# Optimization experiments

Measured on AMD Instinct MI355X. Metric: run time of the kernel, lower is better.

## Reference

```python
import jax, jax.numpy as jnp
import numpy as np

QUALITY = 95
X_MIN, X_MAX = 0.0, 1.0

# JPEG Annex K base quantization tables
_LUMA = np.array([
    [16, 11, 10, 16, 24, 40, 51, 61],
    [12, 12, 14, 19, 26, 58, 60, 55],
    [14, 13, 16, 24, 40, 57, 69, 56],
    [14, 17, 22, 29, 51, 87, 80, 62],
    [18, 22, 37, 56, 68, 109, 103, 77],
    [24, 35, 55, 64, 81, 104, 113, 92],
    [49, 64, 78, 87, 103, 121, 120, 101],
    [72, 92, 95, 98, 112, 100, 103, 99]], dtype=np.float32)
_CHROMA = np.array([
    [17, 18, 24, 47, 99, 99, 99, 99],
    [18, 21, 26, 66, 99, 99, 99, 99],
    [24, 26, 56, 99, 99, 99, 99, 99],
    [47, 66, 99, 99, 99, 99, 99, 99],
    [99, 99, 99, 99, 99, 99, 99, 99],
    [99, 99, 99, 99, 99, 99, 99, 99],
    [99, 99, 99, 99, 99, 99, 99, 99],
    [99, 99, 99, 99, 99, 99, 99, 99]], dtype=np.float32)

def _qtable(base, quality):
    # libjpeg quality scaling (quality >= 50 branch)
    scale = 5000.0 / quality if quality < 50 else 200.0 - 2.0 * quality
    return np.clip(np.floor((base * scale + 50.0) / 100.0), 1.0, 255.0).astype(np.float32)

_QL = jnp.asarray(_qtable(_LUMA, QUALITY))
_QC = jnp.asarray(_qtable(_CHROMA, QUALITY))

# Orthonormal 8x8 DCT-II matrix
_k = np.arange(8)
_D = np.sqrt(2.0 / 8.0) * np.cos((2 * _k[None, :] + 1) * _k[:, None] * np.pi / 16.0)
_D[0, :] /= np.sqrt(2.0)
_D = jnp.asarray(_D.astype(np.float32))

def _jpeg_channel(ch, table):
    """8x8 block DCT -> quantize(round) -> dequantize -> IDCT. ch: [B,H,W] level-shifted."""
    B, H, W = ch.shape
    xb = ch.reshape(B, H // 8, 8, W // 8, 8)
    coef = jnp.einsum('ki,bhiwj,lj->bhkwl', _D, xb, _D)
    t = table[None, None, :, None, :]
    deq = jnp.round(coef / t) * t
    rec = jnp.einsum('ki,bhkwl,lj->bhiwj', _D, deq, _D)
    return rec.reshape(B, H, W)

def _jpeg_roundtrip(x255):
    """x255: [B,H,W,3] float values in [0,255]. Simulates JPEG encode+decode (4:2:0)."""
    r, g, b = x255[..., 0], x255[..., 1], x255[..., 2]
    # JFIF RGB -> YCbCr
    y = 0.299 * r + 0.587 * g + 0.114 * b
    cb = -0.168736 * r - 0.331264 * g + 0.5 * b + 128.0
    cr = 0.5 * r - 0.418688 * g - 0.081312 * b + 128.0
    # Luma at full resolution
    y2 = _jpeg_channel(y - 128.0, _QL) + 128.0
    # Chroma: 2x2 average downsample (4:2:0), codec, nearest upsample
    def down(c):
        B, H, W = c.shape
        return c.reshape(B, H // 2, 2, W // 2, 2).mean(axis=(2, 4))
    def up(c):
        return jnp.repeat(jnp.repeat(c, 2, axis=1), 2, axis=2)
    cb2 = up(_jpeg_channel(down(cb) - 128.0, _QC) + 128.0)
    cr2 = up(_jpeg_channel(down(cr) - 128.0, _QC) + 128.0)
    # YCbCr -> RGB
    r2 = y2 + 1.402 * (cr2 - 128.0)
    g2 = y2 - 0.344136 * (cb2 - 128.0) - 0.714136 * (cr2 - 128.0)
    b2 = y2 + 1.772 * (cb2 - 128.0)
    rgb = jnp.stack([r2, g2, b2], axis=-1)
    return jnp.round(jnp.clip(rgb, 0.0, 255.0))  # decoded uint8 values


def setup_inputs() -> dict:
    key = jax.random.key(0)
    x = jax.random.uniform(key, (32, 512, 512, 3), dtype=jnp.float32)
    return {"x": x}


def reference(x):
    # inputs -> uint8 pixel values (tf.cast truncation; values are >= 0)
    x255 = jnp.clip(jnp.floor((x - X_MIN) / ((X_MAX - X_MIN) / 255.0)), 0.0, 255.0)
    dec = _jpeg_roundtrip(x255)
    # back to input range/dtype
    return dec / (255.0 / (X_MAX - X_MIN)) + X_MIN
```

## Files before the change

### kernel.cpp

```cpp
#include <hip/hip_runtime.h>
#include <cstddef>

static constexpr float D8[8][8] = {
  { 0.35355339059327373f, 0.35355339059327373f, 0.35355339059327373f, 0.35355339059327373f,
    0.35355339059327373f, 0.35355339059327373f, 0.35355339059327373f, 0.35355339059327373f},
  { 0.4903926402016152f,  0.4157348061512726f,  0.27778511650980114f, 0.09754516100806417f,
   -0.09754516100806417f,-0.27778511650980114f,-0.4157348061512726f, -0.4903926402016152f},
  { 0.46193976625564337f, 0.19134171618254492f,-0.19134171618254492f,-0.46193976625564337f,
   -0.46193976625564337f,-0.19134171618254492f, 0.19134171618254492f, 0.46193976625564337f},
  { 0.4157348061512726f, -0.09754516100806417f,-0.4903926402016152f, -0.27778511650980114f,
    0.27778511650980114f, 0.4903926402016152f,  0.09754516100806417f,-0.4157348061512726f},
  { 0.35355339059327373f,-0.35355339059327373f,-0.35355339059327373f, 0.35355339059327373f,
    0.35355339059327373f,-0.35355339059327373f,-0.35355339059327373f, 0.35355339059327373f},
  { 0.27778511650980114f,-0.4903926402016152f,  0.09754516100806417f, 0.4157348061512726f,
   -0.4157348061512726f, -0.09754516100806417f, 0.4903926402016152f, -0.27778511650980114f},
  { 0.19134171618254492f,-0.46193976625564337f, 0.46193976625564337f,-0.19134171618254492f,
   -0.19134171618254492f, 0.46193976625564337f,-0.46193976625564337f, 0.19134171618254492f},
  { 0.09754516100806417f,-0.27778511650980114f, 0.4157348061512726f, -0.4903926402016152f,
    0.4903926402016152f, -0.4157348061512726f,  0.27778511650980114f,-0.09754516100806417f},
};

static constexpr float QLt[8][8] = {
  {2,1,1,2,2,4,5,6},
  {1,1,1,2,3,6,6,6},
  {1,1,2,2,4,6,7,6},
  {1,2,2,3,5,9,8,6},
  {2,2,4,6,7,11,10,8},
  {2,4,6,6,8,10,11,9},
  {5,6,8,9,10,12,12,10},
  {7,9,10,10,11,10,10,10},
};
static constexpr float QCt[8][8] = {
  {2,2,2,5,10,10,10,10},
  {2,2,3,7,10,10,10,10},
  {2,3,6,10,10,10,10,10},
  {5,7,10,10,10,10,10,10},
  {10,10,10,10,10,10,10,10},
  {10,10,10,10,10,10,10,10},
  {10,10,10,10,10,10,10,10},
  {10,10,10,10,10,10,10,10},
};

struct F2 { float q, r; };
struct QTab { F2 v[8][8]; };
static constexpr QTab mkq(const float (&b)[8][8]) {
  QTab t{};
  for (int i = 0; i < 8; ++i)
    for (int j = 0; j < 8; ++j) { t.v[i][j].q = b[i][j]; t.v[i][j].r = 1.0f / b[i][j]; }
  return t;
}
static constexpr QTab QLp = mkq(QLt);
static constexpr QTab QCp = mkq(QCt);

__device__ __forceinline__ void dct8(const float x[8], float u[8]) {
  #pragma unroll
  for (int k = 0; k < 8; ++k) {
    float a = D8[k][0] * x[0];
    #pragma unroll
    for (int j = 1; j < 8; ++j) a += D8[k][j] * x[j];
    u[k] = a;
  }
}

__device__ __forceinline__ void idct8(const float x[8], float u[8]) {
  #pragma unroll
  for (int j = 0; j < 8; ++j) {
    float a = x[0] * D8[0][j];
    #pragma unroll
    for (int m = 1; m < 8; ++m) a += x[m] * D8[m][j];
    u[j] = a;
  }
}

__device__ __forceinline__ float to255(float x) {
  const float c255 = (float)(1.0 / 255.0);
  float y  = x * 255.0f;
  float fl = floorf(y);
  float fr = y - fl;
  if (fr < 2e-4f || fr > 1.0f - 2e-4f) {
    fl = floorf(x / c255);
  }
  return fminf(fmaxf(fl, 0.0f), 255.0f);
}

__device__ __forceinline__ float quant_rt(float u, F2 qp) {
  float tq = u * qp.r;
  float n  = rintf(tq);
  float d  = fabsf(tq - n);
  if (d > 0.499f) {
    n = rintf(u / qp.q);
  }
  return n * qp.q;
}

__global__ __launch_bounds__(256) void jpeg_rt(const float* __restrict__ in,
                                               float* __restrict__ out)
{
  __shared__ __align__(16) float Yp[16][132];
  __shared__ __align__(16) float Cbp[8][68];
  __shared__ __align__(16) float Crp[8][68];
  __shared__ __align__(16) float S1[32][72];
  __shared__ __align__(16) float S2[32][72];
  __shared__ float lut255[256];

  const int t   = threadIdx.x;
  const int tx  = blockIdx.x;
  const int ty  = blockIdx.y;
  const int img = blockIdx.z;

  const int pr = t >> 5;
  const int pc = t & 31;

  lut255[t] = (float)t / 255.0f;

  {
    float yv[2][4];
    float cbv[2][4], crv[2][4];
    #pragma unroll
    for (int rr = 0; rr < 2; ++rr) {
      const size_t grow = (size_t)img * 512 + (size_t)(ty*16 + 2*pr + rr);
      const float* rp = in + (grow*512 + (size_t)(tx*128 + 4*pc))*3;
      float4 A = ((const float4*)rp)[0];
      float4 Bq = ((const float4*)rp)[1];
      float4 Cq = ((const float4*)rp)[2];
      float px[12] = {A.x,A.y,A.z,A.w,Bq.x,Bq.y,Bq.z,Bq.w,Cq.x,Cq.y,Cq.z,Cq.w};
      #pragma unroll
      for (int p = 0; p < 4; ++p) {
        float r = to255(px[3*p+0]);
        float g = to255(px[3*p+1]);
        float b = to255(px[3*p+2]);
        float y  =  0.299f*r + 0.587f*g + 0.114f*b;
        float cb = -0.168736f*r - 0.331264f*g + 0.5f*b + 128.0f;
        float cr =  0.5f*r - 0.418688f*g - 0.081312f*b + 128.0f;
        yv[rr][p]  = y - 128.0f;
        cbv[rr][p] = cb;
        crv[rr][p] = cr;
      }
    }
    *(float4*)&Yp[2*pr+0][4*pc] = make_float4(yv[0][0],yv[0][1],yv[0][2],yv[0][3]);
    *(float4*)&Yp[2*pr+1][4*pc] = make_float4(yv[1][0],yv[1][1],yv[1][2],yv[1][3]);
    float cb0 = ((cbv[0][0]+cbv[0][1]) + (cbv[1][0]+cbv[1][1]))*0.25f - 128.0f;
    float cb1 = ((cbv[0][2]+cbv[0][3]) + (cbv[1][2]+cbv[1][3]))*0.25f - 128.0f;
    float cr0 = ((crv[0][0]+crv[0][1]) + (crv[1][0]+crv[1][1]))*0.25f - 128.0f;
    float cr1 = ((crv[0][2]+crv[0][3]) + (crv[1][2]+crv[1][3]))*0.25f - 128.0f;
    *(float2*)&Cbp[pr][2*pc] = make_float2(cb0, cb1);
    *(float2*)&Crp[pr][2*pc] = make_float2(cr0, cr1);
  }
  __syncthreads();

  {
    const int b = t >> 3, i = t & 7;
    const int br = b >> 4, bc = b & 15;
    const float* src = &Yp[br*8 + i][bc*8];
    float xr[8], u[8];
    *(float4*)&xr[0] = *(const float4*)&src[0];
    *(float4*)&xr[4] = *(const float4*)&src[4];
    dct8(xr, u);
    *(float4*)&S1[b][i*8+0] = make_float4(u[0],u[1],u[2],u[3]);
    *(float4*)&S1[b][i*8+4] = make_float4(u[4],u[5],u[6],u[7]);
  }
  __syncthreads();

  {
    const int b = t >> 3, kk = t & 7;
    float s[8], u[8], v[8];
    #pragma unroll
    for (int i = 0; i < 8; ++i) s[i] = S1[b][i*8 + kk];
    dct8(s, u);
    #pragma unroll
    for (int m = 0; m < 8; ++m) u[m] = quant_rt(u[m], QLp.v[m][kk]);
    idct8(u, v);
    *(float4*)&S2[b][kk*8+0] = make_float4(v[0],v[1],v[2],v[3]);
    *(float4*)&S2[b][kk*8+4] = make_float4(v[4],v[5],v[6],v[7]);
  }
  __syncthreads();

  {
    const int b = t >> 3, j = t & 7;
    float w[8], z[8];
    #pragma unroll
    for (int m = 0; m < 8; ++m) w[m] = S2[b][m*8 + j];
    idct8(w, z);
    const int br = b >> 4, bc = b & 15;
    *(float4*)&Yp[br*8 + j][bc*8 + 0] = make_float4(z[0],z[1],z[2],z[3]);
    *(float4*)&Yp[br*8 + j][bc*8 + 4] = make_float4(z[4],z[5],z[6],z[7]);
  }
  if (t < 128) {
    const int b = t >> 3, i = t & 7;
    const float* plane = (b & 8) ? &Crp[0][0] : &Cbp[0][0];
    const float* src = plane + i*68 + (b & 7)*8;
    float xr[8], u[8];
    *(float4*)&xr[0] = *(const float4*)&src[0];
    *(float4*)&xr[4] = *(const float4*)&src[4];
    dct8(xr, u);
    *(float4*)&S1[b][i*8+0] = make_float4(u[0],u[1],u[2],u[3]);
    *(float4*)&S1[b][i*8+4] = make_float4(u[4],u[5],u[6],u[7]);
  }
  __syncthreads();

  if (t < 128) {
    const int b = t >> 3, kk = t & 7;
    float s[8], u[8], v[8];
    #pragma unroll
    for (int i = 0; i < 8; ++i) s[i] = S1[b][i*8 + kk];
    dct8(s, u);
    #pragma unroll
    for (int m = 0; m < 8; ++m) u[m] = quant_rt(u[m], QCp.v[m][kk]);
    idct8(u, v);
    *(float4*)&S2[b][kk*8+0] = make_float4(v[0],v[1],v[2],v[3]);
    *(float4*)&S2[b][kk*8+4] = make_float4(v[4],v[5],v[6],v[7]);
  }
  __syncthreads();

  if (t < 128) {
    const int b = t >> 3, j = t & 7;
    float w[8], z[8];
    #pragma unroll
    for (int m = 0; m < 8; ++m) w[m] = S2[b][m*8 + j];
    idct8(w, z);
    float* plane = (b & 8) ? &Crp[0][0] : &Cbp[0][0];
    float* dst = plane + j*68 + (b & 7)*8;
    *(float4*)&dst[0] = make_float4(z[0],z[1],z[2],z[3]);
    *(float4*)&dst[4] = make_float4(z[4],z[5],z[6],z[7]);
  }
  __syncthreads();

  {
    float y0[4], y1[4];
    *(float4*)y0 = *(const float4*)&Yp[2*pr+0][4*pc];
    *(float4*)y1 = *(const float4*)&Yp[2*pr+1][4*pc];
    float2 cbp2 = *(const float2*)&Cbp[pr][2*pc];
    float2 crp2 = *(const float2*)&Crp[pr][2*pc];
    float cbq[2] = {cbp2.x, cbp2.y};
    float crq[2] = {crp2.x, crp2.y};
    #pragma unroll
    for (int rr = 0; rr < 2; ++rr) {
      float ov[12];
      #pragma unroll
      for (int p = 0; p < 4; ++p) {
        float y2  = (rr ? y1[p] : y0[p]) + 128.0f;
        float cb2 = cbq[p>>1] + 128.0f;
        float cr2 = crq[p>>1] + 128.0f;
        float r2 = y2 + 1.402f*(cr2 - 128.0f);
        float g2 = y2 - 0.344136f*(cb2 - 128.0f) - 0.714136f*(cr2 - 128.0f);
        float b2 = y2 + 1.772f*(cb2 - 128.0f);
        ov[3*p+0] = lut255[(int)rintf(fminf(fmaxf(r2, 0.0f), 255.0f))];
        ov[3*p+1] = lut255[(int)rintf(fminf(fmaxf(g2, 0.0f), 255.0f))];
        ov[3*p+2] = lut255[(int)rintf(fminf(fmaxf(b2, 0.0f), 255.0f))];
      }
      const size_t grow = (size_t)img * 512 + (size_t)(ty*16 + 2*pr + rr);
      float* op = out + (grow*512 + (size_t)(tx*128 + 4*pc))*3;
      ((float4*)op)[0] = make_float4(ov[0],ov[1],ov[2],ov[3]);
      ((float4*)op)[1] = make_float4(ov[4],ov[5],ov[6],ov[7]);
      ((float4*)op)[2] = make_float4(ov[8],ov[9],ov[10],ov[11]);
    }
  }
}

extern "C" void kernel_launch(void* const* d_in, const int* in_sizes, int n_in,
                              void* d_out, int out_size, void* d_ws, size_t ws_size,
                              hipStream_t stream) {
  (void)in_sizes; (void)n_in; (void)d_ws; (void)ws_size; (void)out_size;
  const float* x = (const float*)d_in[0];
  float* out = (float*)d_out;
  dim3 grid(4, 32, 32);
  jpeg_rt<<<grid, dim3(256), 0, stream>>>(x, out);
}
```

Measured before the change: 189.2 us.

## Merge luma and chroma DCT passes into shared task loops and drop LUT

Luma and chroma 8x8 block transforms now run in unified task loops over 384 row tasks, so the block needs three barriers for the DCT/quantise/IDCT pipeline instead of five, and threads are not left idle while only 128 of them handle chroma. Shared memory is folded into two ping-pong buffers, which lowers LDS use per block and may allow more blocks per CU. The 1/255 lookup table is replaced with a multiply by a reciprocal constant, which can differ from true division in the last bit. Branch hints are also added to the rare exact-rounding fallbacks.

After: 188.0 us. About the same (-0.6%).

```diff
diff --git a/kernel.cpp b/kernel.cpp
--- a/kernel.cpp
+++ b/kernel.cpp
@@ -61,7 +61,6 @@
     u[k] = a;
   }
 }
-
 __device__ __forceinline__ void idct8(const float x[8], float u[8]) {
   #pragma unroll
   for (int j = 0; j < 8; ++j) {
@@ -77,7 +76,7 @@
   float y  = x * 255.0f;
   float fl = floorf(y);
   float fr = y - fl;
-  if (fr < 2e-4f || fr > 1.0f - 2e-4f) {
+  if (__builtin_expect(fr < 2e-4f || fr > 1.0f - 2e-4f, 0)) {
     fl = floorf(x / c255);
   }
   return fminf(fmaxf(fl, 0.0f), 255.0f);
@@ -87,7 +86,7 @@
   float tq = u * qp.r;
   float n  = rintf(tq);
   float d  = fabsf(tq - n);
-  if (d > 0.499f) {
+  if (__builtin_expect(d > 0.499f, 0)) {
     n = rintf(u / qp.q);
   }
   return n * qp.q;
@@ -96,12 +95,8 @@
 __global__ __launch_bounds__(256) void jpeg_rt(const float* __restrict__ in,
                                                float* __restrict__ out)
 {
-  __shared__ __align__(16) float Yp[16][132];
-  __shared__ __align__(16) float Cbp[8][68];
-  __shared__ __align__(16) float Crp[8][68];
-  __shared__ __align__(16) float S1[32][72];
-  __shared__ __align__(16) float S2[32][72];
-  __shared__ float lut255[256];
+  __shared__ __align__(16) float U[3264];
+  __shared__ __align__(16) float V[3264];
 
   const int t   = threadIdx.x;
   const int tx  = blockIdx.x;
@@ -111,11 +106,12 @@
   const int pr = t >> 5;
   const int pc = t & 31;
 
-  lut255[t] = (float)t / 255.0f;
+  float* Yp  = U;
+  float* Cbp = U + 2112;
+  float* Crp = U + 2656;
 
   {
-    float yv[2][4];
-    float cbv[2][4], crv[2][4];
+    float yv[2][4], cbv[2][4], crv[2][4];
     #pragma unroll
     for (int rr = 0; rr < 2; ++rr) {
       const size_t grow = (size_t)img * 512 + (size_t)(ty*16 + 2*pr + rr);
@@ -137,100 +133,79 @@
         crv[rr][p] = cr;
       }
     }
-    *(float4*)&Yp[2*pr+0][4*pc] = make_float4(yv[0][0],yv[0][1],yv[0][2],yv[0][3]);
-    *(float4*)&Yp[2*pr+1][4*pc] = make_float4(yv[1][0],yv[1][1],yv[1][2],yv[1][3]);
+    *(float4*)&Yp[(2*pr+0)*132 + 4*pc] = make_float4(yv[0][0],yv[0][1],yv[0][2],yv[0][3]);
+    *(float4*)&Yp[(2*pr+1)*132 + 4*pc] = make_float4(yv[1][0],yv[1][1],yv[1][2],yv[1][3]);
     float cb0 = ((cbv[0][0]+cbv[0][1]) + (cbv[1][0]+cbv[1][1]))*0.25f - 128.0f;
     float cb1 = ((cbv[0][2]+cbv[0][3]) + (cbv[1][2]+cbv[1][3]))*0.25f - 128.0f;
     float cr0 = ((crv[0][0]+crv[0][1]) + (crv[1][0]+crv[1][1]))*0.25f - 128.0f;
     float cr1 = ((crv[0][2]+crv[0][3]) + (crv[1][2]+crv[1][3]))*0.25f - 128.0f;
-    *(float2*)&Cbp[pr][2*pc] = make_float2(cb0, cb1);
-    *(float2*)&Crp[pr][2*pc] = make_float2(cr0, cr1);
-  }
-  __syncthreads();
-
-  {
-    const int b = t >> 3, i = t & 7;
-    const int br = b >> 4, bc = b & 15;
-    const float* src = &Yp[br*8 + i][bc*8];
+    *(float2*)&Cbp[pr*68 + 2*pc] = make_float2(cb0, cb1);
+    *(float2*)&Crp[pr*68 + 2*pc] = make_float2(cr0, cr1);
+  }
+  __syncthreads();
+
+  #pragma unroll
+  for (int task = t; task < 384; task += 256) {
+    const int tb = task >> 3, i = task & 7;
+    const float* src;
+    if (tb < 32)      src = Yp  + (size_t)((tb>>4)*8 + i)*132 + (tb&15)*8;
+    else if (tb < 40) src = Cbp + i*68 + (tb-32)*8;
+    else              src = Crp + i*68 + (tb-40)*8;
     float xr[8], u[8];
     *(float4*)&xr[0] = *(const float4*)&src[0];
     *(float4*)&xr[4] = *(const float4*)&src[4];
     dct8(xr, u);
-    *(float4*)&S1[b][i*8+0] = make_float4(u[0],u[1],u[2],u[3]);
-    *(float4*)&S1[b][i*8+4] = make_float4(u[4],u[5],u[6],u[7]);
-  }
-  __syncthreads();
-
-  {
-    const int b = t >> 3, kk = t & 7;
+    *(float4*)&V[tb*68 + i*8 + 0] = make_float4(u[0],u[1],u[2],u[3]);
+    *(float4*)&V[tb*68 + i*8 + 4] = make_float4(u[4],u[5],u[6],u[7]);
+  }
+  __syncthreads();
+
+  #pragma unroll
+  for (int task = t; task < 384; task += 256) {
+    const int tb = task >> 3, kk = task & 7;
     float s[8], u[8], v[8];
     #pragma unroll
-    for (int i = 0; i < 8; ++i) s[i] = S1[b][i*8 + kk];
+    for (int i = 0; i < 8; ++i) s[i] = V[tb*68 + i*8 + kk];
     dct8(s, u);
-    #pragma unroll
-    for (int m = 0; m < 8; ++m) u[m] = quant_rt(u[m], QLp.v[m][kk]);
+    if (tb < 32) {
+      #pragma unroll
+      for (int m = 0; m < 8; ++m) u[m] = quant_rt(u[m], QLp.v[m][kk]);
+    } else {
+      #pragma unroll
+      for (int m = 0; m < 8; ++m) u[m] = quant_rt(u[m], QCp.v[m][kk]);
+    }
     idct8(u, v);
-    *(float4*)&S2[b][kk*8+0] = make_float4(v[0],v[1],v[2],v[3]);
-    *(float4*)&S2[b][kk*8+4] = make_float4(v[4],v[5],v[6],v[7]);
-  }
-  __syncthreads();
-
-  {
-    const int b = t >> 3, j = t & 7;
+    *(float4*)&U[tb*68 + kk*8 + 0] = make_float4(v[0],v[1],v[2],v[3]);
+    *(float4*)&U[tb*68 + kk*8 + 4] = make_float4(v[4],v[5],v[6],v[7]);
+  }
+  __syncthreads();
+
+  float* Yr  = V;
+  float* Cbr = V + 2112;
+  float* Crr = V + 2656;
+  #pragma unroll
+  for (int task = t; task < 384; task += 256) {
+    const int tb = task >> 3, j = task & 7;
     float w[8], z[8];
     #pragma unroll
-    for (int m = 0; m < 8; ++m) w[m] = S2[b][m*8 + j];
+    for (int m = 0; m < 8; ++m) w[m] = U[tb*68 + m*8 + j];
     idct8(w, z);
-    const int br = b >> 4, bc = b & 15;
-    *(float4*)&Yp[br*8 + j][bc*8 + 0] = make_float4(z[0],z[1],z[2],z[3]);
-    *(float4*)&Yp[br*8 + j][bc*8 + 4] = make_float4(z[4],z[5],z[6],z[7]);
-  }
-  if (t < 128) {
-    const int b = t >> 3, i = t & 7;
-    const float* plane = (b & 8) ? &Crp[0][0] : &Cbp[0][0];
-    const float* src = plane + i*68 + (b & 7)*8;
-    float xr[8], u[8];
-    *(float4*)&xr[0] = *(const float4*)&src[0];
-    *(float4*)&xr[4] = *(const float4*)&src[4];
-    dct8(xr, u);
-    *(float4*)&S1[b][i*8+0] = make_float4(u[0],u[1],u[2],u[3]);
-    *(float4*)&S1[b][i*8+4] = make_float4(u[4],u[5],u[6],u[7]);
-  }
-  __syncthreads();
-
-  if (t < 128) {
-    const int b = t >> 3, kk = t & 7;
-    float s[8], u[8], v[8];
-    #pragma unroll
-    for (int i = 0; i < 8; ++i) s[i] = S1[b][i*8 + kk];
-    dct8(s, u);
-    #pragma unroll
-    for (int m = 0; m < 8; ++m) u[m] = quant_rt(u[m], QCp.v[m][kk]);
-    idct8(u, v);
-    *(float4*)&S2[b][kk*8+0] = make_float4(v[0],v[1],v[2],v[3]);
-    *(float4*)&S2[b][kk*8+4] = make_float4(v[4],v[5],v[6],v[7]);
-  }
-  __syncthreads();
-
-  if (t < 128) {
-    const int b = t >> 3, j = t & 7;
-    float w[8], z[8];
-    #pragma unroll
-    for (int m = 0; m < 8; ++m) w[m] = S2[b][m*8 + j];
-    idct8(w, z);
-    float* plane = (b & 8) ? &Crp[0][0] : &Cbp[0][0];
-    float* dst = plane + j*68 + (b & 7)*8;
+    float* dst;
+    if (tb < 32)      dst = Yr  + (size_t)((tb>>4)*8 + j)*132 + (tb&15)*8;
+    else if (tb < 40) dst = Cbr + j*68 + (tb-32)*8;
+    else              dst = Crr + j*68 + (tb-40)*8;
     *(float4*)&dst[0] = make_float4(z[0],z[1],z[2],z[3]);
     *(float4*)&dst[4] = make_float4(z[4],z[5],z[6],z[7]);
   }
   __syncthreads();
 
   {
+    const float c255 = (float)(1.0 / 255.0);
     float y0[4], y1[4];
-    *(float4*)y0 = *(const float4*)&Yp[2*pr+0][4*pc];
-    *(float4*)y1 = *(const float4*)&Yp[2*pr+1][4*pc];
-    float2 cbp2 = *(const float2*)&Cbp[pr][2*pc];
-    float2 crp2 = *(const float2*)&Crp[pr][2*pc];
+    *(float4*)y0 = *(const float4*)&Yr[(2*pr+0)*132 + 4*pc];
+    *(float4*)y1 = *(const float4*)&Yr[(2*pr+1)*132 + 4*pc];
+    float2 cbp2 = *(const float2*)&Cbr[pr*68 + 2*pc];
+    float2 crp2 = *(const float2*)&Crr[pr*68 + 2*pc];
     float cbq[2] = {cbp2.x, cbp2.y};
     float crq[2] = {crp2.x, crp2.y};
     #pragma unroll
@@ -244,9 +219,9 @@
         float r2 = y2 + 1.402f*(cr2 - 128.0f);
         float g2 = y2 - 0.344136f*(cb2 - 128.0f) - 0.714136f*(cr2 - 128.0f);
         float b2 = y2 + 1.772f*(cb2 - 128.0f);
-        ov[3*p+0] = lut255[(int)rintf(fminf(fmaxf(r2, 0.0f), 255.0f))];
-        ov[3*p+1] = lut255[(int)rintf(fminf(fmaxf(g2, 0.0f), 255.0f))];
-        ov[3*p+2] = lut255[(int)rintf(fminf(fmaxf(b2, 0.0f), 255.0f))];
+        ov[3*p+0] = rintf(fminf(fmaxf(r2, 0.0f), 255.0f)) * c255;
+        ov[3*p+1] = rintf(fminf(fmaxf(g2, 0.0f), 255.0f)) * c255;
+        ov[3*p+2] = rintf(fminf(fmaxf(b2, 0.0f), 255.0f)) * c255;
       }
       const size_t grow = (size_t)img * 512 + (size_t)(ty*16 + 2*pr + rr);
       float* op = out + (grow*512 + (size_t)(tx*128 + 4*pc))*3;
```
